# Kernel tuning notes

Measured on AMD Instinct MI355X. Metric: run time of the kernel, lower is better.

## Reference

```python
import jax, jax.numpy as jnp
import numpy as np
from jax import lax

N_BOXES = 4000
NUM_CLASSES = 81  # class 0 is background, skipped like the torch loop


def _iou_matrix(boxes):
    # boxes: [N,4] as (x1,y1,x2,y2). Returns [N,N] pairwise IoU.
    x1, y1, x2, y2 = boxes[:, 0], boxes[:, 1], boxes[:, 2], boxes[:, 3]
    area = (x2 - x1) * (y2 - y1)
    ix1 = jnp.maximum(x1[:, None], x1[None, :])
    iy1 = jnp.maximum(y1[:, None], y1[None, :])
    ix2 = jnp.minimum(x2[:, None], x2[None, :])
    iy2 = jnp.minimum(y2[:, None], y2[None, :])
    inter = jnp.clip(ix2 - ix1, 0.0) * jnp.clip(iy2 - iy1, 0.0)
    return inter / (area[:, None] + area[None, :] - inter + 1e-9)


def _nms_keep(iou, score, valid, nms_thresh):
    # Greedy NMS in descending-score order, fixed shape. iou: [N,N].
    n = score.shape[0]
    order = jnp.argsort(-score)
    idx_range = jnp.arange(n)

    def body(i, keep):
        idx = order[i]
        cur = keep[idx]  # still alive -> it suppresses overlapping boxes
        row = iou[idx]
        sup = cur & (row > nms_thresh) & (idx_range != idx)
        return keep & ~sup

    keep = lax.fori_loop(0, n, body, valid)
    return keep & valid


def reference(bboxes, scores, conf_thresh, nms_thresh, max_instances):
    n = bboxes.shape[0]
    iou = _iou_matrix(bboxes)                       # [N,N], shared across classes
    scores_fg = scores[:, 1:].T                     # [C-1, N]
    valid = scores_fg > conf_thresh                 # per-class conf filter
    keep = jax.vmap(lambda s, v: _nms_keep(iou, s, v, nms_thresh))(scores_fg, valid)
    # Kept detections get their score; everything else -1 (padding sentinel).
    final = jnp.where(keep, scores_fg, -1.0)        # [C-1, N]
    top_vals, top_idx = lax.top_k(final.reshape(-1), max_instances)
    cls = top_idx // n                              # label = class_index - 1 (0-based fg)
    box_idx = top_idx % n
    preds = jnp.concatenate([bboxes[box_idx], top_vals[:, None]], axis=1)  # [K,5]
    valid_out = top_vals > 0.0
    preds = jnp.where(valid_out[:, None], preds, 0.0)
    labels = jnp.where(valid_out, cls, -1)
    return preds, labels


def setup_inputs() -> dict:
    key = jax.random.key(0)
    k1, k2, k3 = jax.random.split(key, 3)
    cxcy = jax.random.uniform(k1, (N_BOXES, 2), dtype=jnp.float32) * 1000.0
    wh = jax.random.uniform(k2, (N_BOXES, 2), dtype=jnp.float32) * 100.0 + 1.0
    bboxes = jnp.concatenate([cxcy - wh * 0.5, cxcy + wh * 0.5], axis=1)
    scores = jax.random.uniform(k3, (N_BOXES, NUM_CLASSES), dtype=jnp.float32)
    return {
        "bboxes": bboxes,
        "scores": scores,
        "conf_thresh": jnp.float32(0.5),
        "nms_thresh": jnp.float32(0.5),
        "max_instances": 100,
    }
```

## Files before the change

### kernel.cpp

```cpp
#include <hip/hip_runtime.h>
#include <stdint.h>

typedef unsigned long long u64;
typedef unsigned int u32;

#define NB    4000
#define NCLS  80
#define ROWW  64
#define MAXI  100
#define NKEY  (NCLS * MAXI)
#define PCAP  4096
#define SMAX  4096
#define NSEG  8
#define SEGN  (NKEY / NSEG)
#define SELT  448
#define NTH   512

__device__ __forceinline__ u32 mono_f32(float f) {
    u32 u = __float_as_uint(f);
    return (u & 0x80000000u) ? ~u : (u | 0x80000000u);
}

__device__ __forceinline__ void find_cross(const u32* hist, int T, int lane,
                                           int* outB, int* outA) {
    int running = 0, B = -1, A = 0;
    for (int g = 0; g < 16 && B < 0; ++g) {
        const int d = 1023 - (g * 64 + lane);
        const int cnt = (int)hist[d];
        int pre = cnt;
        #pragma unroll
        for (int off = 1; off < 64; off <<= 1) {
            const int v = __shfl_up(pre, off);
            if (lane >= off) pre += v;
        }
        const int incl = running + pre;
        const int excl = incl - cnt;
        const u64 hm = __ballot(excl < T && incl >= T);
        if (hm != 0ull) {
            const int hl = (int)__builtin_ctzll(hm);
            B = __shfl(d, hl);
            A = __shfl(excl, hl);
        }
        running = __shfl(incl, 63);
    }
    *outB = B; *outA = A;
}

__global__ __launch_bounds__(256) void k_suppr(const float4* __restrict__ boxes,
                                               const float* __restrict__ nms_t,
                                               u64* __restrict__ suppr,
                                               int* __restrict__ zero_region) {
    if (blockIdx.x == 0) {
        for (int i = threadIdx.x; i < NCLS + NKEY; i += 256) zero_region[i] = 0;
    }
    const int i0  = blockIdx.x * 4;
    const int tid = threadIdx.x;
    const float t = *nms_t;
    float4 bi[4]; float ai[4];
    #pragma unroll
    for (int r = 0; r < 4; ++r) {
        bi[r] = boxes[i0 + r];
        ai[r] = (bi[r].z - bi[r].x) * (bi[r].w - bi[r].y);
    }
    #pragma unroll
    for (int ch = 0; ch < 16; ++ch) {
        const int j = ch * 256 + tid;
        const bool inb = (j < NB);
        float4 bj = make_float4(0.f, 0.f, 0.f, 0.f);
        float aj = 0.f;
        if (inb) { bj = boxes[j]; aj = (bj.z - bj.x) * (bj.w - bj.y); }
        #pragma unroll
        for (int r = 0; r < 4; ++r) {
            bool bit = false;
            if (inb && j != i0 + r) {
                const float ix1 = fmaxf(bi[r].x, bj.x), iy1 = fmaxf(bi[r].y, bj.y);
                const float ix2 = fminf(bi[r].z, bj.z), iy2 = fminf(bi[r].w, bj.w);
                const float inter = fmaxf(ix2 - ix1, 0.0f) * fmaxf(iy2 - iy1, 0.0f);
                bit = inter / (ai[r] + aj - inter + 1e-9f) > t;
            }
            const u64 m = __ballot(bit);
            if ((tid & 63) == 0) suppr[(size_t)(i0 + r) * ROWW + (j >> 6)] = m;
        }
    }
}

__global__ __launch_bounds__(256) void k_compact(const float* __restrict__ scores,
                                                 const float* __restrict__ conf_t,
                                                 u64* __restrict__ pkeys,
                                                 int* __restrict__ gcnt) {
    const int b    = blockIdx.x * 256 + threadIdx.x;
    const int c    = blockIdx.y;
    const int wid  = threadIdx.x >> 6;
    const int lane = threadIdx.x & 63;
    __shared__ int wcnt[4];
    __shared__ int bbase;
    const float conf = *conf_t;
    const bool inb = (b < NB);
    const float s = inb ? scores[b * 81 + c + 1] : -1e30f;
    const bool valid = inb && (s > conf);
    const u64 mask = __ballot(valid);
    if (lane == 0) wcnt[wid] = (int)__popcll(mask);
    __syncthreads();
    if (threadIdx.x == 0) {
        const int t0 = wcnt[0], t1 = wcnt[1], t2 = wcnt[2], t3 = wcnt[3];
        const int tot = t0 + t1 + t2 + t3;
        bbase = tot ? atomicAdd(&gcnt[c], tot) : 0;
        wcnt[0] = 0; wcnt[1] = t0; wcnt[2] = t0 + t1; wcnt[3] = t0 + t1 + t2;
    }
    __syncthreads();
    if (valid) {
        const int off = (int)__popcll(mask & ((1ull << lane) - 1ull));
        pkeys[c * PCAP + bbase + wcnt[wid] + off] =
            ((u64)mono_f32(s) << 32) | (u64)(0xFFFFFFFFu - (u32)b);
    }
}

__global__ __launch_bounds__(NTH) void k_classnms(const u64* __restrict__ pkeys,
                                                  const int* __restrict__ gcnt,
                                                  const u64* __restrict__ suppr,
                                                  u64* __restrict__ cand) {
    __shared__ u64 skey[SMAX];
    __shared__ unsigned short sbox[SMAX];
    __shared__ int sh_kept, sh_M, sh_B, sh_A, sh_B2;

    u32* hist = (u32*)sbox;

    const int c    = blockIdx.x;
    const int tid  = threadIdx.x;
    const int lane = tid & 63;

    const int nvalid = gcnt[c];

    u64 own[8];
    #pragma unroll
    for (int q = 0; q < 8; ++q) {
        const int idx = tid + q * NTH;
        own[q] = (idx < nvalid) ? pkeys[c * PCAP + idx] : 0ull;
    }

    bool full = (nvalid <= 512);
    int kept = 0;

    for (int attempt = 0; attempt < 2; ++attempt) {
        int M;
        if (!full) {
            for (int i = tid; i < 1024; i += NTH) hist[i] = 0;
            if (tid == 0) sh_M = 0;
            __syncthreads();
            #pragma unroll
            for (int q = 0; q < 8; ++q)
                if (tid + q * NTH < nvalid)
                    atomicAdd(&hist[(u32)(own[q] >> 54) & 1023u], 1u);
            __syncthreads();
            if (tid < 64) {
                int B, A;
                find_cross(hist, SELT, lane, &B, &A);
                if (lane == 0) { sh_B = B; sh_A = A; }
            }
            __syncthreads();
            const int B = sh_B, A = sh_A;
            for (int i = tid; i < 1024; i += NTH) hist[i] = 0;
            __syncthreads();
            #pragma unroll
            for (int q = 0; q < 8; ++q)
                if (tid + q * NTH < nvalid &&
                    ((u32)(own[q] >> 54) & 1023u) == (u32)B)
                    atomicAdd(&hist[(u32)(own[q] >> 44) & 1023u], 1u);
            __syncthreads();
            if (tid < 64) {
                int B2, A2;
                find_cross(hist, SELT - A, lane, &B2, &A2);
                if (lane == 0) sh_B2 = B2;
            }
            __syncthreads();
            const int B2 = sh_B2;
            #pragma unroll
            for (int q = 0; q < 8; ++q) {
                bool sel = false;
                if (tid + q * NTH < nvalid) {
                    const int d = (int)((u32)(own[q] >> 54) & 1023u);
                    sel = (d > B) ||
                          (d == B && (int)((u32)(own[q] >> 44) & 1023u) >= B2);
                }
                const u64 bm = __ballot(sel);
                int wbase = 0;
                if (lane == 0 && bm) wbase = atomicAdd(&sh_M, (int)__popcll(bm));
                wbase = __shfl(wbase, 0);
                if (sel)
                    skey[wbase + (int)__popcll(bm & ((1ull << lane) - 1ull))] = own[q];
            }
            __syncthreads();
            M = sh_M;
        } else {
            #pragma unroll
            for (int q = 0; q < 8; ++q) {
                const int idx = tid + q * NTH;
                if (idx < nvalid) skey[idx] = own[q];
            }
            M = nvalid;
            __syncthreads();
        }

        int S = 64;
        while (S < M) S <<= 1;
        for (int i = M + tid; i < S; i += NTH) skey[i] = 0;
        __syncthreads();

        for (int k2 = 2; k2 <= S; k2 <<= 1) {
            for (int j = k2 >> 1; j >= 64; j >>= 1) {
                for (int p = tid; p < (S >> 1); p += NTH) {
                    const int i0 = ((p & ~(j - 1)) << 1) | (p & (j - 1));
                    const u64 a = skey[i0], b = skey[i0 | j];
                    const bool up = ((i0 & k2) == 0);
                    if (up ? (a < b) : (a > b)) { skey[i0] = b; skey[i0 | j] = a; }
                }
                __syncthreads();
            }
            for (int base = 0; base < S; base += NTH) {
                const int i = base + tid;
                if (i < S) {
                    u64 x = skey[i];
                    #pragma unroll
                    for (int j2 = 32; j2 >= 1; j2 >>= 1) {
                        if (j2 < k2) {
                            const u64 y = __shfl_xor(x, j2);
                            const bool wantmax = (((i & k2) == 0) == ((i & j2) == 0));
                            x = wantmax ? (x > y ? x : y) : (x < y ? x : y);
                        }
                    }
                    skey[i] = x;
                }
            }
            __syncthreads();
        }

        for (int i = tid; i < S; i += NTH)
            sbox[i] = (unsigned short)(0xFFFFFFFFu - (u32)skey[i]);
        __syncthreads();

        if (tid < 64) {
            u64 keptmask = 0;
            int kp = 0;
            if (M > 0) {
                const int last = M - 1;
                u64 wA[16], wB[16];
                #pragma unroll
                for (int q = 0; q < 16; ++q) {
                    const int idx = (q <= last) ? q : last;
                    wA[q] = suppr[(size_t)sbox[idx] * ROWW + lane];
                }
                for (int cs = 0; cs < M && kp < MAXI; cs += 32) {
                    #pragma unroll
                    for (int q = 0; q < 16; ++q) {
                        const int want = cs + 16 + q;
                        const int idx = (want <= last) ? want : last;
                        wB[q] = suppr[(size_t)sbox[idx] * ROWW + lane];
                    }
                    #pragma unroll
                    for (int q = 0; q < 16; ++q) {
                        const int p = cs + q;
                        if (p < M && kp < MAXI) {
                            const bool sup = (__ballot((wA[q] & keptmask) != 0ull) != 0ull);
                            if (!sup) {
                                const int b = sbox[p];
                                if (lane == (b >> 6)) keptmask |= (1ull << (b & 63));
                                if (lane == 0) {
                                    const u32 mono = (u32)(skey[p] >> 32);
                                    const u32 flat = (u32)(c * NB + b);
                                    cand[c * MAXI + kp] =
                                        ((u64)mono << 32) | (u64)(0xFFFFFFFFu - flat);
                                }
                                kp++;
                            }
                        }
                    }
                    #pragma unroll
                    for (int q = 0; q < 16; ++q) {
                        const int want = cs + 32 + q;
                        const int idx = (want <= last) ? want : last;
                        wA[q] = suppr[(size_t)sbox[idx] * ROWW + lane];
                    }
                    #pragma unroll
                    for (int q = 0; q < 16; ++q) {
                        const int p = cs + 16 + q;
                        if (p < M && kp < MAXI) {
                            const bool sup = (__ballot((wB[q] & keptmask) != 0ull) != 0ull);
                            if (!sup) {
                                const int b = sbox[p];
                                if (lane == (b >> 6)) keptmask |= (1ull << (b & 63));
                                if (lane == 0) {
                                    const u32 mono = (u32)(skey[p] >> 32);
                                    const u32 flat = (u32)(c * NB + b);
                                    cand[c * MAXI + kp] =
                                        ((u64)mono << 32) | (u64)(0xFFFFFFFFu - flat);
                                }
                                kp++;
                            }
                        }
                    }
                }
            }
            if (lane == 0) sh_kept = kp;
        }
        __syncthreads();
        kept = sh_kept;

        if (kept >= MAXI || full) break;
        full = true;
    }

    for (int s = tid; s < MAXI; s += NTH)
        if (s >= kept) cand[c * MAXI + s] = 0;
}

__global__ __launch_bounds__(256) void k_rankseg(const u64* __restrict__ cand,
                                                 int* __restrict__ grank) {
    __shared__ u64 keys[SEGN];
    const int s   = blockIdx.x;
    const int c   = blockIdx.y;
    const int tid = threadIdx.x;

    for (int i = tid; i < SEGN; i += 256) keys[i] = cand[s * SEGN + i];
    __syncthreads();

    if (tid < 2 * MAXI) {
        const int ci   = tid >> 1;
        const int half = tid & 1;
        const u64 mine = cand[c * MAXI + ci];
        if (mine != 0ull) {
            int cnt = 0;
            const int beg = half * (SEGN / 2), end = beg + (SEGN / 2);
            #pragma unroll 4
            for (int m = beg; m < end; ++m) cnt += (keys[m] > mine);
            cnt += __shfl_xor(cnt, 1);
            if (half == 0 && cnt > 0) atomicAdd(&grank[c * MAXI + ci], cnt);
        }
    }
}

__global__ __launch_bounds__(1024) void k_emit(const u64* __restrict__ cand,
                                               const int* __restrict__ grank,
                                               const float4* __restrict__ boxes,
                                               float* __restrict__ out) {
    const int tid = threadIdx.x;
    if (tid < MAXI) {
        out[tid*5+0] = 0.0f; out[tid*5+1] = 0.0f; out[tid*5+2] = 0.0f;
        out[tid*5+3] = 0.0f; out[tid*5+4] = 0.0f;
        out[500 + tid] = -1.0f;
    }
    __syncthreads();
    for (int i = tid; i < NKEY; i += 1024) {
        const u64 k = cand[i];
        if (k == 0ull) continue;
        const int r = grank[i];
        if (r >= MAXI) continue;
        const u32 mono = (u32)(k >> 32);
        const float sc  = __uint_as_float(mono ^ 0x80000000u);
        const u32 flat = 0xFFFFFFFFu - (u32)k;
        const int b    = (int)(flat % NB);
        const float4 bb = boxes[b];
        out[r*5+0] = bb.x; out[r*5+1] = bb.y;
        out[r*5+2] = bb.z; out[r*5+3] = bb.w;
        out[r*5+4] = sc;
        out[500 + r] = (float)(flat / NB);
    }
}

extern "C" void kernel_launch(void* const* d_in, const int* in_sizes, int n_in,
                              void* d_out, int out_size, void* d_ws, size_t ws_size,
                              hipStream_t stream) {
    const float4* bboxes = (const float4*)d_in[0];
    const float*  scores = (const float*)d_in[1];
    const float*  conf_t = (const float*)d_in[2];
    const float*  nms_t  = (const float*)d_in[3];

    char* ws = (char*)d_ws;
    u64* suppr = (u64*)ws;
    u64* pkeys = (u64*)(ws + 2048000);
    u64* cand  = (u64*)(ws + 2048000 + 2621440);
    int* gcnt  = (int*)(ws + 2048000 + 2621440 + 64000);
    int* grank = (int*)(ws + 2048000 + 2621440 + 64000 + 320);

    k_suppr<<<NB / 4, 256, 0, stream>>>(bboxes, nms_t, suppr, gcnt);
    k_compact<<<dim3(16, NCLS), 256, 0, stream>>>(scores, conf_t, pkeys, gcnt);
    k_classnms<<<NCLS, NTH, 0, stream>>>(pkeys, gcnt, suppr, cand);
    k_rankseg<<<dim3(NSEG, NCLS), 256, 0, stream>>>(cand, grank);
    k_emit<<<1, 1024, 0, stream>>>(cand, grank, bboxes, (float*)d_out);
}
```

Before: 135.7 us.

## Fuse pre-pass kernels, drop atomic compaction, replace rank/emit with radix top-k

Merges the IoU suppression-mask and score-key kernels into one launch. Keys are now written densely per class with zero as the invalid marker, so the global atomic counters and the zeroing pass are no longer needed. The class-NMS kernel counts valid keys itself and compacts them into shared memory. The two-kernel global rank and emit stage becomes a single-block radix select that narrows the candidates to at most 256, then ranks them in shared memory. This cuts the pipeline from five launches to three and shortens the serial tail, at the cost of a denser pkeys read and extra radix passes in one block.

```diff
diff --git a/kernel.cpp b/kernel.cpp
--- a/kernel.cpp
+++ b/kernel.cpp
@@ -5,14 +5,12 @@
 typedef unsigned int u32;
 
 #define NB    4000
+#define NBP   4096
 #define NCLS  80
 #define ROWW  64
 #define MAXI  100
 #define NKEY  (NCLS * MAXI)
-#define PCAP  4096
 #define SMAX  4096
-#define NSEG  8
-#define SEGN  (NKEY / NSEG)
 #define SELT  448
 #define NTH   512
 
@@ -46,97 +44,91 @@
     *outB = B; *outA = A;
 }
 
-__global__ __launch_bounds__(256) void k_suppr(const float4* __restrict__ boxes,
-                                               const float* __restrict__ nms_t,
-                                               u64* __restrict__ suppr,
-                                               int* __restrict__ zero_region) {
-    if (blockIdx.x == 0) {
-        for (int i = threadIdx.x; i < NCLS + NKEY; i += 256) zero_region[i] = 0;
-    }
-    const int i0  = blockIdx.x * 4;
+__global__ __launch_bounds__(256) void k_pre(const float4* __restrict__ boxes,
+                                             const float* __restrict__ scores,
+                                             const float* __restrict__ conf_t,
+                                             const float* __restrict__ nms_t,
+                                             u64* __restrict__ suppr,
+                                             u64* __restrict__ pkeys) {
     const int tid = threadIdx.x;
-    const float t = *nms_t;
-    float4 bi[4]; float ai[4];
-    #pragma unroll
-    for (int r = 0; r < 4; ++r) {
-        bi[r] = boxes[i0 + r];
-        ai[r] = (bi[r].z - bi[r].x) * (bi[r].w - bi[r].y);
-    }
-    #pragma unroll
-    for (int ch = 0; ch < 16; ++ch) {
-        const int j = ch * 256 + tid;
-        const bool inb = (j < NB);
-        float4 bj = make_float4(0.f, 0.f, 0.f, 0.f);
-        float aj = 0.f;
-        if (inb) { bj = boxes[j]; aj = (bj.z - bj.x) * (bj.w - bj.y); }
+    if (blockIdx.x < NB / 4) {
+        const int i0  = blockIdx.x * 4;
+        const float t = *nms_t;
+        float4 bi[4]; float ai[4];
         #pragma unroll
         for (int r = 0; r < 4; ++r) {
-            bool bit = false;
-            if (inb && j != i0 + r) {
-                const float ix1 = fmaxf(bi[r].x, bj.x), iy1 = fmaxf(bi[r].y, bj.y);
-                const float ix2 = fminf(bi[r].z, bj.z), iy2 = fminf(bi[r].w, bj.w);
-                const float inter = fmaxf(ix2 - ix1, 0.0f) * fmaxf(iy2 - iy1, 0.0f);
-                bit = inter / (ai[r] + aj - inter + 1e-9f) > t;
-            }
-            const u64 m = __ballot(bit);
-            if ((tid & 63) == 0) suppr[(size_t)(i0 + r) * ROWW + (j >> 6)] = m;
-        }
-    }
-}
-
-__global__ __launch_bounds__(256) void k_compact(const float* __restrict__ scores,
-                                                 const float* __restrict__ conf_t,
-                                                 u64* __restrict__ pkeys,
-                                                 int* __restrict__ gcnt) {
-    const int b    = blockIdx.x * 256 + threadIdx.x;
-    const int c    = blockIdx.y;
-    const int wid  = threadIdx.x >> 6;
-    const int lane = threadIdx.x & 63;
-    __shared__ int wcnt[4];
-    __shared__ int bbase;
-    const float conf = *conf_t;
-    const bool inb = (b < NB);
-    const float s = inb ? scores[b * 81 + c + 1] : -1e30f;
-    const bool valid = inb && (s > conf);
-    const u64 mask = __ballot(valid);
-    if (lane == 0) wcnt[wid] = (int)__popcll(mask);
-    __syncthreads();
-    if (threadIdx.x == 0) {
-        const int t0 = wcnt[0], t1 = wcnt[1], t2 = wcnt[2], t3 = wcnt[3];
-        const int tot = t0 + t1 + t2 + t3;
-        bbase = tot ? atomicAdd(&gcnt[c], tot) : 0;
-        wcnt[0] = 0; wcnt[1] = t0; wcnt[2] = t0 + t1; wcnt[3] = t0 + t1 + t2;
-    }
-    __syncthreads();
-    if (valid) {
-        const int off = (int)__popcll(mask & ((1ull << lane) - 1ull));
-        pkeys[c * PCAP + bbase + wcnt[wid] + off] =
-            ((u64)mono_f32(s) << 32) | (u64)(0xFFFFFFFFu - (u32)b);
+            bi[r] = boxes[i0 + r];
+            ai[r] = (bi[r].z - bi[r].x) * (bi[r].w - bi[r].y);
+        }
+        #pragma unroll
+        for (int ch = 0; ch < 16; ++ch) {
+            const int j = ch * 256 + tid;
+            const bool inb = (j < NB);
+            float4 bj = make_float4(0.f, 0.f, 0.f, 0.f);
+            float aj = 0.f;
+            if (inb) { bj = boxes[j]; aj = (bj.z - bj.x) * (bj.w - bj.y); }
+            #pragma unroll
+            for (int r = 0; r < 4; ++r) {
+                bool bit = false;
+                if (inb && j != i0 + r) {
+                    const float ix1 = fmaxf(bi[r].x, bj.x), iy1 = fmaxf(bi[r].y, bj.y);
+                    const float ix2 = fminf(bi[r].z, bj.z), iy2 = fminf(bi[r].w, bj.w);
+                    const float inter = fmaxf(ix2 - ix1, 0.0f) * fmaxf(iy2 - iy1, 0.0f);
+                    bit = inter / (ai[r] + aj - inter + 1e-9f) > t;
+                }
+                const u64 m = __ballot(bit);
+                if ((tid & 63) == 0) suppr[(size_t)(i0 + r) * ROWW + (j >> 6)] = m;
+            }
+        }
+    } else {
+        const int idx = blockIdx.x - NB / 4;
+        const int c   = idx >> 4;
+        const int b   = ((idx & 15) << 8) | tid;
+        const float conf = *conf_t;
+        u64 key = 0;
+        if (b < NB) {
+            const float s = scores[b * 81 + c + 1];
+            if (s > conf)
+                key = ((u64)mono_f32(s) << 32) | (u64)(0xFFFFFFFFu - (u32)b);
+        }
+        pkeys[c * NBP + b] = key;
     }
 }
 
 __global__ __launch_bounds__(NTH) void k_classnms(const u64* __restrict__ pkeys,
-                                                  const int* __restrict__ gcnt,
                                                   const u64* __restrict__ suppr,
                                                   u64* __restrict__ cand) {
     __shared__ u64 skey[SMAX];
     __shared__ unsigned short sbox[SMAX];
-    __shared__ int sh_kept, sh_M, sh_B, sh_A, sh_B2;
+    __shared__ int wsum[8];
+    __shared__ int sh_kept, sh_M, sh_B, sh_A, sh_B2, sh_nvalid;
 
     u32* hist = (u32*)sbox;
 
     const int c    = blockIdx.x;
     const int tid  = threadIdx.x;
     const int lane = tid & 63;
-
-    const int nvalid = gcnt[c];
+    const int wid  = tid >> 6;
 
     u64 own[8];
+    int cnt = 0;
     #pragma unroll
     for (int q = 0; q < 8; ++q) {
-        const int idx = tid + q * NTH;
-        own[q] = (idx < nvalid) ? pkeys[c * PCAP + idx] : 0ull;
-    }
+        own[q] = pkeys[c * NBP + tid + q * NTH];
+        cnt += (own[q] != 0ull);
+    }
+    #pragma unroll
+    for (int off = 1; off < 64; off <<= 1) cnt += __shfl_xor(cnt, off);
+    if (lane == 0) wsum[wid] = cnt;
+    __syncthreads();
+    if (tid == 0) {
+        int t = 0;
+        #pragma unroll
+        for (int w = 0; w < 8; ++w) t += wsum[w];
+        sh_nvalid = t;
+    }
+    __syncthreads();
+    const int nvalid = sh_nvalid;
 
     bool full = (nvalid <= 512);
     int kept = 0;
@@ -149,7 +141,7 @@
             __syncthreads();
             #pragma unroll
             for (int q = 0; q < 8; ++q)
-                if (tid + q * NTH < nvalid)
+                if (own[q] != 0ull)
                     atomicAdd(&hist[(u32)(own[q] >> 54) & 1023u], 1u);
             __syncthreads();
             if (tid < 64) {
@@ -163,8 +155,7 @@
             __syncthreads();
             #pragma unroll
             for (int q = 0; q < 8; ++q)
-                if (tid + q * NTH < nvalid &&
-                    ((u32)(own[q] >> 54) & 1023u) == (u32)B)
+                if (own[q] != 0ull && ((u32)(own[q] >> 54) & 1023u) == (u32)B)
                     atomicAdd(&hist[(u32)(own[q] >> 44) & 1023u], 1u);
             __syncthreads();
             if (tid < 64) {
@@ -177,7 +168,7 @@
             #pragma unroll
             for (int q = 0; q < 8; ++q) {
                 bool sel = false;
-                if (tid + q * NTH < nvalid) {
+                if (own[q] != 0ull) {
                     const int d = (int)((u32)(own[q] >> 54) & 1023u);
                     sel = (d > B) ||
                           (d == B && (int)((u32)(own[q] >> 44) & 1023u) >= B2);
@@ -192,13 +183,20 @@
             __syncthreads();
             M = sh_M;
         } else {
+            if (tid == 0) sh_M = 0;
+            __syncthreads();
             #pragma unroll
             for (int q = 0; q < 8; ++q) {
-                const int idx = tid + q * NTH;
-                if (idx < nvalid) skey[idx] = own[q];
-            }
-            M = nvalid;
-            __syncthreads();
+                const bool sel = (own[q] != 0ull);
+                const u64 bm = __ballot(sel);
+                int wbase = 0;
+                if (lane == 0 && bm) wbase = atomicAdd(&sh_M, (int)__popcll(bm));
+                wbase = __shfl(wbase, 0);
+                if (sel)
+                    skey[wbase + (int)__popcll(bm & ((1ull << lane) - 1ull))] = own[q];
+            }
+            __syncthreads();
+            M = sh_M;
         }
 
         int S = 64;
@@ -313,56 +311,108 @@
         if (s >= kept) cand[c * MAXI + s] = 0;
 }
 
-__global__ __launch_bounds__(256) void k_rankseg(const u64* __restrict__ cand,
-                                                 int* __restrict__ grank) {
-    __shared__ u64 keys[SEGN];
-    const int s   = blockIdx.x;
-    const int c   = blockIdx.y;
-    const int tid = threadIdx.x;
-
-    for (int i = tid; i < SEGN; i += 256) keys[i] = cand[s * SEGN + i];
+__global__ __launch_bounds__(1024) void k_final(const u64* __restrict__ cand,
+                                                const float4* __restrict__ boxes,
+                                                float* __restrict__ out) {
+    __shared__ u32 hist[1024];
+    __shared__ u64 sel[256];
+    __shared__ int wsum[16];
+    __shared__ int sh_total, sh_A, sh_B, sh_bits, sh_M, sh_cnt;
+    __shared__ u64 sh_prefix;
+
+    const int tid  = threadIdx.x;
+    const int lane = tid & 63;
+    const int wid  = tid >> 6;
+
+    u64 myk[8];
+    int cnt = 0;
+    #pragma unroll
+    for (int q = 0; q < 8; ++q) {
+        const int i = tid + (q << 10);
+        myk[q] = (i < NKEY) ? cand[i] : 0ull;
+        cnt += (myk[q] != 0ull);
+    }
+    #pragma unroll
+    for (int off = 1; off < 64; off <<= 1) cnt += __shfl_xor(cnt, off);
+    if (lane == 0) wsum[wid] = cnt;
+    if (tid < 256) sel[tid] = 0;
     __syncthreads();
-
-    if (tid < 2 * MAXI) {
-        const int ci   = tid >> 1;
-        const int half = tid & 1;
-        const u64 mine = cand[c * MAXI + ci];
-        if (mine != 0ull) {
-            int cnt = 0;
-            const int beg = half * (SEGN / 2), end = beg + (SEGN / 2);
-            #pragma unroll 4
-            for (int m = beg; m < end; ++m) cnt += (keys[m] > mine);
-            cnt += __shfl_xor(cnt, 1);
-            if (half == 0 && cnt > 0) atomicAdd(&grank[c * MAXI + ci], cnt);
-        }
-    }
-}
-
-__global__ __launch_bounds__(1024) void k_emit(const u64* __restrict__ cand,
-                                               const int* __restrict__ grank,
-                                               const float4* __restrict__ boxes,
-                                               float* __restrict__ out) {
-    const int tid = threadIdx.x;
+    if (tid == 0) {
+        int t = 0;
+        #pragma unroll
+        for (int w = 0; w < 16; ++w) t += wsum[w];
+        sh_total = t; sh_A = 0; sh_bits = 0; sh_prefix = 0; sh_cnt = 0;
+    }
+    __syncthreads();
+    const int total = sh_total;
+    const int Tt = (total < MAXI) ? total : MAXI;
+
+    if (total > 0) {
+        for (int lvl = 0; lvl < 6; ++lvl) {
+            hist[tid & 1023] = 0;
+            __syncthreads();
+            const int bits = sh_bits;
+            const u64 pref = sh_prefix;
+            const int shift = 54 - bits;
+            #pragma unroll
+            for (int q = 0; q < 8; ++q) {
+                const u64 k = myk[q];
+                if (k != 0ull && (bits == 0 || (k >> (64 - bits)) == pref))
+                    atomicAdd(&hist[(u32)(k >> shift) & 1023u], 1u);
+            }
+            __syncthreads();
+            if (tid < 64) {
+                const int T = Tt - sh_A;
+                int B, A;
+                find_cross(hist, T, lane, &B, &A);
+                if (lane == 0) { sh_B = B; sh_A += A; }
+            }
+            __syncthreads();
+            if (tid == 0) {
+                sh_M = sh_A + (int)hist[sh_B];
+                sh_prefix = (sh_prefix << 10) | (u32)sh_B;
+                sh_bits += 10;
+            }
+            __syncthreads();
+            if (sh_M <= 256) break;
+        }
+        const int bits = sh_bits;
+        const u64 pref = sh_prefix;
+        #pragma unroll
+        for (int q = 0; q < 8; ++q) {
+            const u64 k = myk[q];
+            const bool s = (k != 0ull) && ((k >> (64 - bits)) >= pref);
+            const u64 bm = __ballot(s);
+            int wbase = 0;
+            if (lane == 0 && bm) wbase = atomicAdd(&sh_cnt, (int)__popcll(bm));
+            wbase = __shfl(wbase, 0);
+            if (s) sel[wbase + (int)__popcll(bm & ((1ull << lane) - 1ull))] = k;
+        }
+    }
+
     if (tid < MAXI) {
         out[tid*5+0] = 0.0f; out[tid*5+1] = 0.0f; out[tid*5+2] = 0.0f;
         out[tid*5+3] = 0.0f; out[tid*5+4] = 0.0f;
         out[500 + tid] = -1.0f;
     }
     __syncthreads();
-    for (int i = tid; i < NKEY; i += 1024) {
-        const u64 k = cand[i];
-        if (k == 0ull) continue;
-        const int r = grank[i];
-        if (r >= MAXI) continue;
-        const u32 mono = (u32)(k >> 32);
-        const float sc  = __uint_as_float(mono ^ 0x80000000u);
-        const u32 flat = 0xFFFFFFFFu - (u32)k;
-        const int b    = (int)(flat % NB);
-        const float4 bb = boxes[b];
-        out[r*5+0] = bb.x; out[r*5+1] = bb.y;
-        out[r*5+2] = bb.z; out[r*5+3] = bb.w;
-        out[r*5+4] = sc;
-        out[500 + r] = (float)(flat / NB);
+    if (tid < 256) {
+        const u64 my = sel[tid];
+        if (my != 0ull) {
+            int r = 0;
+            for (int j = 0; j < 256; ++j) r += (sel[j] > my);
+            if (r < MAXI) {
+                const u32 mono = (u32)(my >> 32);
+                const float sc = __uint_as_float(mono ^ 0x80000000u);
+                const u32 flat = 0xFFFFFFFFu - (u32)my;
+                const int b    = (int)(flat % NB);
+                const float4 bb = boxes[b];
+                out[r*5+0] = bb.x; out[r*5+1] = bb.y;
+                out[r*5+2] = bb.z; out[r*5+3] = bb.w;
+                out[r*5+4] = sc;
+                out[500 + r] = (float)(flat / NB);
+            }
+        }
     }
 }
 
@@ -378,12 +428,9 @@
     u64* suppr = (u64*)ws;
     u64* pkeys = (u64*)(ws + 2048000);
     u64* cand  = (u64*)(ws + 2048000 + 2621440);
-    int* gcnt  = (int*)(ws + 2048000 + 2621440 + 64000);
-    int* grank = (int*)(ws + 2048000 + 2621440 + 64000 + 320);
-
-    k_suppr<<<NB / 4, 256, 0, stream>>>(bboxes, nms_t, suppr, gcnt);
-    k_compact<<<dim3(16, NCLS), 256, 0, stream>>>(scores, conf_t, pkeys, gcnt);
-    k_classnms<<<NCLS, NTH, 0, stream>>>(pkeys, gcnt, suppr, cand);
-    k_rankseg<<<dim3(NSEG, NCLS), 256, 0, stream>>>(cand, grank);
-    k_emit<<<1, 1024, 0, stream>>>(cand, grank, bboxes, (float*)d_out);
-}
+
+    k_pre<<<NB / 4 + 16 * NCLS, 256, 0, stream>>>(bboxes, scores, conf_t, nms_t,
+                                                  suppr, pkeys);
+    k_classnms<<<NCLS, NTH, 0, stream>>>(pkeys, suppr, cand);
+    k_final<<<1, 1024, 0, stream>>>(cand, bboxes, (float*)d_out);
+}
```

Result: faster. 124.3 us (-8.4%).
